# Performance work log

Hardware: AMD Instinct MI355X
Metric: run time of the kernel (lower is better)

The kernel has to match this reference:

```python
import jax, jax.numpy as jnp
import numpy as np

B, S = 1, 2048
D, HD, NH, NKV, L, V, FF = 2048, 256, 8, 4, 4, 32000, 8192
WINDOW = 1024
SOFTCAP = 50.0
FINAL_CAP = 30.0
EPS = 1e-6
THETA = 10000.0
ATTN_TYPES = ("local", "global", "local", "global")
NEG = -2.3819763e38
SCALE = HD ** -0.5


def _rms(x, w):
    # RMSNorm with unit offset: x * rsqrt(mean(x^2)+eps) * (1 + w)
    n = x * jax.lax.rsqrt(jnp.mean(x * x, axis=-1, keepdims=True) + EPS)
    return n * (1.0 + w)


def _rope(x, cos, sin):
    # x: [B, S, H, HD]; rotate-half formulation (Gemma pairs i with i+HD/2)
    h = HD // 2
    x1, x2 = x[..., :h], x[..., h:]
    c = cos[None, :, None, :]
    s = sin[None, :, None, :]
    return jnp.concatenate([x1 * c - x2 * s, x1 * s + x2 * c], axis=-1)


def setup_inputs() -> dict:
    key = jax.random.key(0)
    ks = jax.random.split(key, 15)
    sd = 0.02
    f = lambda k, shape: jax.random.normal(k, shape, jnp.float32) * sd
    return {
        "input_ids": jax.random.randint(ks[0], (B, S), 0, V),
        "embed": f(ks[1], (V, D)),
        "wq": f(ks[2], (L, NH * HD, D)),
        "wk": f(ks[3], (L, NKV * HD, D)),
        "wv": f(ks[4], (L, NKV * HD, D)),
        "wo": f(ks[5], (L, D, NH * HD)),
        "wg": f(ks[6], (L, FF, D)),
        "wu": f(ks[7], (L, FF, D)),
        "wd": f(ks[8], (L, D, FF)),
        "ln_in": f(ks[9], (L, D)),
        "ln_pa": f(ks[10], (L, D)),
        "ln_pf": f(ks[11], (L, D)),
        "ln_pff": f(ks[12], (L, D)),
        "ln_f": f(ks[13], (D,)),
        "w_lm": f(ks[14], (V, D)),
    }


def _forward(input_ids, embed, wq, wk, wv, wo, wg, wu, wd,
             ln_in, ln_pa, ln_pf, ln_pff, ln_f, w_lm):
    # rotary tables
    pos = jnp.arange(S, dtype=jnp.float32)
    inv = 1.0 / (THETA ** (jnp.arange(0, HD, 2, dtype=jnp.float32) / HD))
    ang = pos[:, None] * inv[None, :]
    cos, sin = jnp.cos(ang), jnp.sin(ang)  # [S, HD/2]

    # additive masks
    i = jnp.arange(S)[:, None]
    j = jnp.arange(S)[None, :]
    causal = jnp.where(j > i, NEG, 0.0).astype(jnp.float32)
    local = jnp.where((j > i) | (i - j >= WINDOW), NEG, 0.0).astype(jnp.float32)

    h = embed[input_ids] * jnp.asarray(D ** 0.5, jnp.float32)
    rep = NH // NKV
    for l in range(L):
        mask = local if ATTN_TYPES[l] == "local" else causal
        x = _rms(h, ln_in[l])
        q = jnp.einsum('bsd,od->bso', x, wq[l]).reshape(B, S, NH, HD)
        k = jnp.einsum('bsd,od->bso', x, wk[l]).reshape(B, S, NKV, HD)
        v = jnp.einsum('bsd,od->bso', x, wv[l]).reshape(B, S, NKV, HD)
        q = _rope(q, cos, sin)
        k = _rope(k, cos, sin)
        k = jnp.repeat(k, rep, axis=2)  # GQA expand
        v = jnp.repeat(v, rep, axis=2)
        q = q.transpose(0, 2, 1, 3)  # bhsd
        k = k.transpose(0, 2, 1, 3)
        v = v.transpose(0, 2, 1, 3)
        qk = jnp.einsum('bhsd,bhfd->bhsf', q, k) * SCALE
        qk = jnp.tanh(qk / SOFTCAP) * SOFTCAP  # attn logit softcap
        scores = jax.nn.softmax(qk + mask, axis=-1)
        a = jnp.einsum('bhsf,bhfd->bhsd', scores, v)
        a = a.transpose(0, 2, 1, 3).reshape(B, S, NH * HD)
        attn_out = jnp.einsum('bso,do->bsd', a, wo[l])
        h = h + _rms(attn_out, ln_pa[l])  # post-attn norm then residual
        x = _rms(h, ln_pf[l])
        gate = jax.nn.gelu(jnp.einsum('bsd,fd->bsf', x, wg[l]), approximate=True)
        up = jnp.einsum('bsd,fd->bsf', x, wu[l])
        mlp = jnp.einsum('bsf,df->bsd', gate * up, wd[l])
        h = h + _rms(mlp, ln_pff[l])
    h = _rms(h, ln_f)
    logits = jnp.einsum('bsd,vd->bsv', h, w_lm)
    return jnp.tanh(logits / FINAL_CAP) * FINAL_CAP


def reference(input_ids, embed, wq, wk, wv, wo, wg, wu, wd,
              ln_in, ln_pa, ln_pf, ln_pff, ln_f, w_lm):
    return _forward(input_ids, embed, wq, wk, wv, wo, wg, wu, wd,
                    ln_in, ln_pa, ln_pf, ln_pff, ln_f, w_lm)
```

## Files before the change

### kernel.cpp

```cpp
#include <hip/hip_runtime.h>
#include <hip/hip_bf16.h>

typedef __attribute__((ext_vector_type(8))) __bf16 bf16x8;
typedef __attribute__((ext_vector_type(4))) float floatx4;

typedef __attribute__((address_space(1))) const unsigned char kGlb;
typedef __attribute__((address_space(3))) unsigned char kLds;

static constexpr int S = 2048;
static constexpr int D = 2048;
static constexpr int HD = 256;
static constexpr int NH = 8;
static constexpr int NKV = 4;
static constexpr int NLAYER = 4;
static constexpr int VOCAB = 32000;
static constexpr int FF = 8192;
static constexpr int WINDOW = 1024;

__device__ __forceinline__ float blk_sum(float v) {
    __shared__ float sm[4];
    #pragma unroll
    for (int o = 32; o > 0; o >>= 1) v += __shfl_down(v, o, 64);
    int lane = threadIdx.x & 63, w = threadIdx.x >> 6;
    __syncthreads();
    if (lane == 0) sm[w] = v;
    __syncthreads();
    return sm[0] + sm[1] + sm[2] + sm[3];
}

__device__ __forceinline__ float blk_max(float v) {
    __shared__ float sm[4];
    #pragma unroll
    for (int o = 32; o > 0; o >>= 1) v = fmaxf(v, __shfl_down(v, o, 64));
    int lane = threadIdx.x & 63, w = threadIdx.x >> 6;
    __syncthreads();
    if (lane == 0) sm[w] = v;
    __syncthreads();
    return fmaxf(fmaxf(sm[0], sm[1]), fmaxf(sm[2], sm[3]));
}

__global__ void embed_kernel(const int* __restrict__ ids, const float* __restrict__ E,
                             float* __restrict__ h) {
    int d = blockIdx.x * 256 + threadIdx.x;
    int s = blockIdx.y;
    h[(long)s * D + d] = E[(long)ids[s] * D + d] * 45.25483399593904f;
}

__global__ void rope_table_kernel(float* __restrict__ c, float* __restrict__ sn) {
    int i = threadIdx.x;
    int p = blockIdx.x;
    float inv = powf(10000.f, -(float)i / 128.f);
    float a = (float)p * inv;
    c[p * 128 + i] = cosf(a);
    sn[p * 128 + i] = sinf(a);
}

__global__ void cvt_bf16_kernel(const float* __restrict__ src, __hip_bfloat16* __restrict__ dst,
                                long n8) {
    long stride = (long)gridDim.x * 256;
    for (long i = (long)blockIdx.x * 256 + threadIdx.x; i < n8; i += stride) {
        long o = i * 8;
        float4 a = *(const float4*)(src + o);
        float4 b = *(const float4*)(src + o + 4);
        __hip_bfloat16 h8[8] = {
            __float2bfloat16(a.x), __float2bfloat16(a.y),
            __float2bfloat16(a.z), __float2bfloat16(a.w),
            __float2bfloat16(b.x), __float2bfloat16(b.y),
            __float2bfloat16(b.z), __float2bfloat16(b.w)};
        *(uint4*)(dst + o) = *(const uint4*)h8;
    }
}

__global__ void cvt_inter_kernel(const float* __restrict__ src, __hip_bfloat16* __restrict__ dst,
                                 int half, long n8) {
    long stride = (long)gridDim.x * 256;
    for (long i = (long)blockIdx.x * 256 + threadIdx.x; i < n8; i += stride) {
        long o = i * 8;
        long row = o >> 11, col = o & 2047;
        float4 a = *(const float4*)(src + o);
        float4 b = *(const float4*)(src + o + 4);
        __hip_bfloat16 h8[8] = {
            __float2bfloat16(a.x), __float2bfloat16(a.y),
            __float2bfloat16(a.z), __float2bfloat16(a.w),
            __float2bfloat16(b.x), __float2bfloat16(b.y),
            __float2bfloat16(b.z), __float2bfloat16(b.w)};
        *(uint4*)(dst + ((row * 2 + half) << 11) + col) = *(const uint4*)h8;
    }
}

__global__ void rms_bf16_kernel(const float* __restrict__ h, const float* __restrict__ w,
                                __hip_bfloat16* __restrict__ o) {
    int s = blockIdx.x;
    const float* row = h + (long)s * D;
    float vals[8], ss = 0.f;
    #pragma unroll
    for (int t = 0; t < 8; ++t) {
        int j = t * 256 + threadIdx.x;
        float v = row[j]; vals[t] = v; ss += v * v;
    }
    ss = blk_sum(ss);
    float r = rsqrtf(ss * (1.f / D) + 1e-6f);
    #pragma unroll
    for (int t = 0; t < 8; ++t) {
        int j = t * 256 + threadIdx.x;
        o[(long)s * D + j] = __float2bfloat16(vals[t] * r * (1.f + w[j]));
    }
}

__global__ void resid_rms_kernel(float* __restrict__ h, const float* __restrict__ tt,
                                 const float* __restrict__ w) {
    int s = blockIdx.x;
    const float* row = tt + (long)s * D;
    float* hr = h + (long)s * D;
    float vals[8], ss = 0.f;
    #pragma unroll
    for (int t = 0; t < 8; ++t) {
        int j = t * 256 + threadIdx.x;
        float v = row[j]; vals[t] = v; ss += v * v;
    }
    ss = blk_sum(ss);
    float r = rsqrtf(ss * (1.f / D) + 1e-6f);
    #pragma unroll
    for (int t = 0; t < 8; ++t) {
        int j = t * 256 + threadIdx.x;
        hr[j] += vals[t] * r * (1.f + w[j]);
    }
}

__global__ void rope_kernel(__hip_bfloat16* __restrict__ x, const float* __restrict__ cb,
                            const float* __restrict__ sb, int ldx) {
    int s = blockIdx.x, hh = blockIdx.y, i = threadIdx.x;
    __hip_bfloat16* p = x + (long)s * ldx + hh * HD;
    float x1 = __bfloat162float(p[i]);
    float x2 = __bfloat162float(p[128 + i]);
    float c = cb[s * 128 + i], sn = sb[s * 128 + i];
    p[i]       = __float2bfloat16(x1 * c - x2 * sn);
    p[128 + i] = __float2bfloat16(x1 * sn + x2 * c);
}

__global__ void transpose_v_kernel(const __hip_bfloat16* __restrict__ v,
                                   __hip_bfloat16* __restrict__ vt, int ldv) {
    __shared__ ushort tile[64][65];
    int s0 = blockIdx.x * 64, d0 = blockIdx.y * 64, kv = blockIdx.z;
    const ushort* vin = (const ushort*)v;
    ushort* vout = (ushort*)vt;
    #pragma unroll
    for (int it = 0; it < 4; ++it) {
        int slot = it * 256 + threadIdx.x;
        int r = slot >> 4, c4 = (slot & 15) << 2;
        ushort4 x = *(const ushort4*)(vin + (long)(s0 + r) * ldv + kv * HD + d0 + c4);
        tile[r][c4] = x.x; tile[r][c4 + 1] = x.y; tile[r][c4 + 2] = x.z; tile[r][c4 + 3] = x.w;
    }
    __syncthreads();
    #pragma unroll
    for (int it = 0; it < 4; ++it) {
        int slot = it * 256 + threadIdx.x;
        int rr = slot >> 4, c4 = (slot & 15) << 2;
        ushort4 y;
        y.x = tile[c4][rr]; y.y = tile[c4 + 1][rr]; y.z = tile[c4 + 2][rr]; y.w = tile[c4 + 3][rr];
        *(ushort4*)(vout + (long)kv * HD * S + (long)(d0 + rr) * S + s0 + c4) = y;
    }
}

__global__ void softmax_kernel(const __hip_bfloat16* __restrict__ sc,
                               __hip_bfloat16* __restrict__ pr, int isLocal) {
    int i = blockIdx.x, hh = blockIdx.y;
    const __hip_bfloat16* row = sc + ((long)hh * S + i) * S;
    __hip_bfloat16* orow = pr + ((long)hh * S + i) * S;
    int lo = isLocal ? max(0, i - (WINDOW - 1)) : 0;
    float vals[8];
    float m = -3.0e38f;
    #pragma unroll
    for (int t = 0; t < 8; ++t) {
        int j = t * 256 + threadIdx.x;
        bool chunkAny = (t * 256 <= i) && (t * 256 + 255 >= lo);
        if (chunkAny) {
            bool valid = (j <= i) && (j >= lo);
            float v = tanhf(__bfloat162float(row[j]) * (0.0625f / 50.f)) * 50.f;
            vals[t] = valid ? v : -3.0e38f;
            m = fmaxf(m, vals[t]);
        } else {
            vals[t] = -3.0e38f;
        }
    }
    m = blk_max(m);
    float ps[8], ssum = 0.f;
    #pragma unroll
    for (int t = 0; t < 8; ++t) {
        float p = (vals[t] > -1.0e38f) ? __expf(vals[t] - m) : 0.f;
        ps[t] = p; ssum += p;
    }
    ssum = blk_sum(ssum);
    float inv = 1.f / ssum;
    #pragma unroll
    for (int t = 0; t < 8; ++t) {
        int j = t * 256 + threadIdx.x;
        orow[j] = __float2bfloat16(ps[t] * inv);
    }
}

__global__ void mul_gu_kernel(__hip_bfloat16* __restrict__ gu) {
    long idx = ((long)blockIdx.x * 256 + threadIdx.x) * 8;
    long s = idx >> 13;
    long f = idx & 8191;
    __hip_bfloat16* gp = gu + s * 16384 + f;
    const __hip_bfloat16* up = gu + s * 16384 + 8192 + f;
    uint4 gv = *(const uint4*)gp;
    uint4 uv = *(const uint4*)up;
    const __hip_bfloat16* gb = (const __hip_bfloat16*)&gv;
    const __hip_bfloat16* ub = (const __hip_bfloat16*)&uv;
    __hip_bfloat16 o[8];
    #pragma unroll
    for (int j = 0; j < 8; ++j)
        o[j] = __float2bfloat16(__bfloat162float(gb[j]) * __bfloat162float(ub[j]));
    *(uint4*)gp = *(const uint4*)o;
}

template<int EPI, int WM, int WN, int MI, int NI>
__global__ __launch_bounds__(WM*WN*64, 2) void gemm_pipe(
    const __hip_bfloat16* __restrict__ A, const __hip_bfloat16* __restrict__ B,
    void* __restrict__ Cv, int K, int lda, int ldb, int ldc,
    long aBatch, long bBatch, long cBatch, int bzDiv, int gx, int kMode) {
    constexpr int T  = WM * WN * 64;
    constexpr int BM = WM * MI * 16;
    constexpr int BN = WN * NI * 16;
    constexpr int AE = BM * 32;
    constexpr int BE = BN * 32;
    __shared__ __hip_bfloat16 lds[4][AE + BE];

    const int tid = threadIdx.x;
    const int nwg = gridDim.x;
    const int orig = blockIdx.x;
    const int wgid = (orig & 7) * (nwg >> 3) + (orig >> 3);
    const int bx = wgid % gx, by = wgid / gx;
    const int bz = blockIdx.z;

    int kstart = 0, kend = K;
    if (kMode == 1) { if (by > bx) return; }
    else if (kMode == 2) { if (by > bx || bx - by >= 9) return; }
    else if (kMode == 3) { kend = min(K, (bx + 1) * BM); }
    else if (kMode == 4) { kend = min(K, (bx + 1) * BM); kstart = max(0, (bx - 1024 / BM) * BM); }

    const __hip_bfloat16* Ab = A + (long)bz * aBatch + (long)bx * BM * lda;
    const __hip_bfloat16* Bb = B + (long)(bz / bzDiv) * bBatch + (long)by * BN * ldb;

    const int w = tid >> 6, l = tid & 63;
    const int wm = w / WN, wn = w % WN;
    const int wrow = wm * MI * 16, wcol = wn * NI * 16;
    const int fr = l & 15, g = l >> 4;
    const int sR = tid >> 2;
    const int sc = tid & 3;

    floatx4 acc[MI][NI] = {};
    bf16x8 bfv[NI];
    bf16x8 af[MI / 2];

    auto stageA = [&](int t, int buf) {
        const int k0 = kstart + t * 32;
        #pragma unroll
        for (int i = 0; i < 2; ++i) {
            int row = sR + i * (T / 4);
            int scol = ((sc ^ ((row >> 1) & 3)) << 3);
            __builtin_amdgcn_global_load_lds(
                (kGlb*)(Ab + (long)row * lda + k0 + scol),
                (kLds*)(&lds[buf][0] + tid * 8 + i * (T * 8)), 16, 0, 0);
        }
    };
    auto stageB = [&](int t, int buf) {
        const int k0 = kstart + t * 32;
        #pragma unroll
        for (int i = 0; i < 2; ++i) {
            int row = sR + i * (T / 4);
            int scol = ((sc ^ ((row >> 1) & 3)) << 3);
            __builtin_amdgcn_global_load_lds(
                (kGlb*)(Bb + (long)row * ldb + k0 + scol),
                (kLds*)(&lds[buf][AE] + tid * 8 + i * (T * 8)), 16, 0, 0);
        }
    };

    auto phase0 = [&](int buf, int t3, bool doStage) {
        const char* AsB = (const char*)&lds[buf][0];
        const char* BsB = (const char*)&lds[buf][AE];
        #pragma unroll
        for (int mi = 0; mi < MI / 2; ++mi) {
            int ra = wrow + mi * 16 + fr;
            af[mi] = *(const bf16x8*)(AsB + ra * 64 + ((g ^ ((ra >> 1) & 3)) << 4));
        }
        #pragma unroll
        for (int ni = 0; ni < NI; ++ni) {
            int rb = wcol + ni * 16 + fr;
            bfv[ni] = *(const bf16x8*)(BsB + rb * 64 + ((g ^ ((rb >> 1) & 3)) << 4));
        }
        if (doStage) stageA(t3, t3 & 3);
        __builtin_amdgcn_s_barrier();
        asm volatile("s_waitcnt lgkmcnt(0)" ::: "memory");
        __builtin_amdgcn_sched_barrier(0);
        __builtin_amdgcn_s_setprio(1);
        #pragma unroll
        for (int mi = 0; mi < MI / 2; ++mi)
            #pragma unroll
            for (int ni = 0; ni < NI; ++ni)
                acc[mi][ni] = __builtin_amdgcn_mfma_f32_16x16x32_bf16(af[mi], bfv[ni], acc[mi][ni], 0, 0, 0);
        __builtin_amdgcn_s_setprio(0);
        __builtin_amdgcn_sched_barrier(0);
        __builtin_amdgcn_s_barrier();
    };

    auto phase1 = [&](int buf, int t3, bool doStage, int vm) {
        const char* AsB = (const char*)&lds[buf][0];
        #pragma unroll
        for (int mi = 0; mi < MI / 2; ++mi) {
            int ra = wrow + (MI / 2 + mi) * 16 + fr;
            af[mi] = *(const bf16x8*)(AsB + ra * 64 + ((g ^ ((ra >> 1) & 3)) << 4));
        }
        if (doStage) stageB(t3, t3 & 3);
        if (vm == 8)      asm volatile("s_waitcnt vmcnt(8)" ::: "memory");
        else if (vm == 4) asm volatile("s_waitcnt vmcnt(4)" ::: "memory");
        else if (vm == 0) asm volatile("s_waitcnt vmcnt(0)" ::: "memory");
        __builtin_amdgcn_s_barrier();
        asm volatile("s_waitcnt lgkmcnt(0)" ::: "memory");
        __builtin_amdgcn_sched_barrier(0);
        __builtin_amdgcn_s_setprio(1);
        #pragma unroll
        for (int mi = 0; mi < MI / 2; ++mi)
            #pragma unroll
            for (int ni = 0; ni < NI; ++ni)
                acc[MI / 2 + mi][ni] = __builtin_amdgcn_mfma_f32_16x16x32_bf16(af[mi], bfv[ni], acc[MI / 2 + mi][ni], 0, 0, 0);
        __builtin_amdgcn_s_setprio(0);
        __builtin_amdgcn_sched_barrier(0);
        __builtin_amdgcn_s_barrier();
    };

    const int nt = (kend - kstart) >> 5;
    stageA(0, 0); stageB(0, 0);
    stageA(1, 1); stageB(1, 1);
    stageA(2, 2); stageB(2, 2);
    asm volatile("s_waitcnt vmcnt(8)" ::: "memory");
    __builtin_amdgcn_s_barrier();

    for (int t = 0; t < nt - 3; ++t) {
        const int b = t & 3;
        phase0(b, t + 3, true);
        phase1(b, t + 3, true, 8);
    }
    phase0((nt - 3) & 3, 0, false); phase1((nt - 3) & 3, 0, false, 4);
    phase0((nt - 2) & 3, 0, false); phase1((nt - 2) & 3, 0, false, 0);
    phase0((nt - 1) & 3, 0, false); phase1((nt - 1) & 3, 0, false, -1);

    const long cBase = (long)bz * cBatch + (long)bx * BM * ldc + (long)by * BN;
    const int rg = (l >> 4) * 4;
    #pragma unroll
    for (int mi = 0; mi < MI; ++mi) {
        #pragma unroll
        for (int ni = 0; ni < NI; ++ni) {
            #pragma unroll
            for (int r = 0; r < 4; ++r) {
                int row = wrow + mi * 16 + rg + r;
                int col = wcol + ni * 16 + fr;
                float v = acc[mi][ni][r];
                if constexpr (EPI == 5) {
                    float pv = __shfl_xor(v, 1);
                    if (!(fr & 1)) {
                        float gg = 0.5f * v * (1.f + tanhf(0.7978845608f * (v + 0.044715f * v * v * v)));
                        long idx5 = ((long)bx * BM + row) * (long)ldc + (long)by * (BN / 2) + (col >> 1);
                        ((__hip_bfloat16*)Cv)[idx5] = __float2bfloat16(gg * pv);
                    }
                } else {
                    long idx = cBase + (long)row * ldc + col;
                    if constexpr (EPI == 0) {
                        ((float*)Cv)[idx] = v;
                    } else if constexpr (EPI == 1) {
                        ((__hip_bfloat16*)Cv)[idx] = __float2bfloat16(v);
                    } else if constexpr (EPI == 3) {
                        ((float*)Cv)[idx] = tanhf(v * (1.f / 30.f)) * 30.f;
                    }
                }
            }
        }
    }
}

template<int EPI>
__global__ __launch_bounds__(256) void gemm_f32w(
    const __hip_bfloat16* __restrict__ A, const float* __restrict__ Bv,
    void* __restrict__ Cv, int K, int lda, int ldb, int ldc) {
    __shared__ __hip_bfloat16 As[128][32];
    __shared__ __hip_bfloat16 Bs[128][32];
    const int tid = threadIdx.x;
    const __hip_bfloat16* Ab = A + (long)blockIdx.x * 128 * lda;
    const float* Bb = Bv + (long)blockIdx.y * 128 * ldb;
    const int wid = tid >> 6, lane = tid & 63;
    const int wr = (wid >> 1) * 64, wc = (wid & 1) * 64;
    const int fr = lane & 15;
    const int kb = (lane >> 4) * 8;
    floatx4 acc[4][4] = {};
    for (int k0 = 0; k0 < K; k0 += 32) {
        __syncthreads();
        #pragma unroll
        for (int it = 0; it < 2; ++it) {
            int slot = tid + it * 256;
            int r = slot >> 2, c8 = (slot & 3) * 8;
            *reinterpret_cast<uint4*>(&As[r][c8]) =
                *reinterpret_cast<const uint4*>(Ab + (long)r * lda + k0 + c8);
        }
        #pragma unroll
        for (int it = 0; it < 4; ++it) {
            int slot = tid + it * 256;
            int r = slot >> 3, c4 = (slot & 7) * 4;
            float4 f = *reinterpret_cast<const float4*>(Bb + (long)r * ldb + k0 + c4);
            __hip_bfloat16 t4[4] = {__float2bfloat16(f.x), __float2bfloat16(f.y),
                                    __float2bfloat16(f.z), __float2bfloat16(f.w)};
            *reinterpret_cast<ushort4*>(&Bs[r][c4]) = *reinterpret_cast<const ushort4*>(t4);
        }
        __syncthreads();
        bf16x8 af[4], bfr[4];
        #pragma unroll
        for (int i = 0; i < 4; ++i)
            af[i] = *reinterpret_cast<const bf16x8*>(&As[wr + i * 16 + fr][kb]);
        #pragma unroll
        for (int j = 0; j < 4; ++j)
            bfr[j] = *reinterpret_cast<const bf16x8*>(&Bs[wc + j * 16 + fr][kb]);
        #pragma unroll
        for (int i = 0; i < 4; ++i)
            #pragma unroll
            for (int j = 0; j < 4; ++j)
                acc[i][j] = __builtin_amdgcn_mfma_f32_16x16x32_bf16(af[i], bfr[j], acc[i][j], 0, 0, 0);
    }
    const long cTile = (long)blockIdx.x * 128 * ldc + (long)blockIdx.y * 128;
    const int rg = (lane >> 4) * 4;
    #pragma unroll
    for (int i = 0; i < 4; ++i)
        #pragma unroll
        for (int j = 0; j < 4; ++j)
            #pragma unroll
            for (int r = 0; r < 4; ++r) {
                int row = wr + i * 16 + rg + r;
                int col = wc + j * 16 + fr;
                long idx = cTile + (long)row * ldc + col;
                float v = acc[i][j][r];
                if constexpr (EPI == 0) ((float*)Cv)[idx] = v;
                else if constexpr (EPI == 1) ((__hip_bfloat16*)Cv)[idx] = __float2bfloat16(v);
                else if constexpr (EPI == 2) {
                    float gg = 0.5f * v * (1.f + tanhf(0.7978845608f * (v + 0.044715f * v * v * v)));
                    ((__hip_bfloat16*)Cv)[idx] = __float2bfloat16(gg);
                } else ((float*)Cv)[idx] = tanhf(v * (1.f / 30.f)) * 30.f;
            }
}

extern "C" void kernel_launch(void* const* d_in, const int* in_sizes, int n_in,
                              void* d_out, int out_size, void* d_ws, size_t ws_size,
                              hipStream_t stream) {
    const int*   ids    = (const int*)d_in[0];
    const float* embedW = (const float*)d_in[1];
    const float* wq     = (const float*)d_in[2];
    const float* wk     = (const float*)d_in[3];
    const float* wv     = (const float*)d_in[4];
    const float* wo     = (const float*)d_in[5];
    const float* wg     = (const float*)d_in[6];
    const float* wu     = (const float*)d_in[7];
    const float* wd     = (const float*)d_in[8];
    const float* ln_in  = (const float*)d_in[9];
    const float* ln_pa  = (const float*)d_in[10];
    const float* ln_pf  = (const float*)d_in[11];
    const float* ln_pff = (const float*)d_in[12];
    const float* ln_f   = (const float*)d_in[13];
    const float* w_lm   = (const float*)d_in[14];
    float* out = (float*)d_out;

    char* ws = (char*)d_ws;
    size_t off = 0;
    auto alloc = [&](size_t bytes) -> void* {
        size_t o = (off + 255) & ~(size_t)255;
        off = o + bytes;
        return (void*)(ws + o);
    };

    float* h            = (float*)alloc((size_t)S * D * 4);
    __hip_bfloat16* xb  = (__hip_bfloat16*)alloc((size_t)S * D * 2);
    __hip_bfloat16* qkvb = (__hip_bfloat16*)alloc((size_t)S * 4096 * 2);
    __hip_bfloat16* vT  = (__hip_bfloat16*)alloc((size_t)NKV * HD * S * 2);
    __hip_bfloat16* ab  = (__hip_bfloat16*)alloc((size_t)S * NH * HD * 2);
    float* tmpf         = (float*)alloc((size_t)S * D * 4);
    __hip_bfloat16* guP = (__hip_bfloat16*)alloc((size_t)S * FF * 2);
    __hip_bfloat16* gu  = (__hip_bfloat16*)alloc((size_t)S * 16384 * 2);
    float* cosb         = (float*)alloc((size_t)S * 128 * 4);
    float* sinb         = (float*)alloc((size_t)S * 128 * 4);
    __hip_bfloat16* scores = (__hip_bfloat16*)alloc((size_t)NH * S * S * 2);
    __hip_bfloat16* probs  = (__hip_bfloat16*)alloc((size_t)NH * S * S * 2);

    const long SLq = 2048L * 2048, SLkv = 1024L * 2048, SLff = 8192L * 2048;
    const long nWlm = (long)VOCAB * D;
    __hip_bfloat16* wqkvb = (__hip_bfloat16*)alloc(4L * 4096 * 2048 * 2);
    __hip_bfloat16* wgub  = (__hip_bfloat16*)alloc(4L * 16384 * 2048 * 2);
    __hip_bfloat16* wob   = (__hip_bfloat16*)alloc(4L * SLq * 2);
    __hip_bfloat16* wdb   = (__hip_bfloat16*)alloc(4L * SLff * 2);
    __hip_bfloat16* wlmb  = (__hip_bfloat16*)alloc(nWlm * 2);
    const bool big = (off <= ws_size);
    (void)in_sizes; (void)n_in; (void)out_size;

    rope_table_kernel<<<dim3(S), dim3(128), 0, stream>>>(cosb, sinb);
    embed_kernel<<<dim3(D / 256, S), dim3(256), 0, stream>>>(ids, embedW, h);

    auto cvt = [&](const float* s, __hip_bfloat16* dp, long n) {
        long n8 = n / 8;
        long want = (n8 + 255) / 256;
        int blocks = (int)(want < 2048 ? want : 2048);
        cvt_bf16_kernel<<<dim3(blocks), dim3(256), 0, stream>>>(s, dp, n8);
    };
    auto cvtI = [&](const float* s, __hip_bfloat16* dp, int half, long n) {
        long n8 = n / 8;
        long want = (n8 + 255) / 256;
        int blocks = (int)(want < 2048 ? want : 2048);
        cvt_inter_kernel<<<dim3(blocks), dim3(256), 0, stream>>>(s, dp, half, n8);
    };
    if (big) {
        for (int l = 0; l < NLAYER; ++l) {
            cvt(wq + l * SLq,  wqkvb + (size_t)l * 4096 * 2048,                SLq);
            cvt(wk + l * SLkv, wqkvb + (size_t)l * 4096 * 2048 + 2048L * 2048, SLkv);
            cvt(wv + l * SLkv, wqkvb + (size_t)l * 4096 * 2048 + 3072L * 2048, SLkv);
            cvtI(wg + l * SLff, wgub + (size_t)l * 16384 * 2048, 0, SLff);
            cvtI(wu + l * SLff, wgub + (size_t)l * 16384 * 2048, 1, SLff);
        }
        cvt(wo, wob, 4L * SLq);
        cvt(wd, wdb, 4L * SLff);
        cvt(w_lm, wlmb, nWlm);
    }

    auto p256 = [&](int epi, const __hip_bfloat16* A, const __hip_bfloat16* B, void* C,
                    int K, int lda, int ldb, int ldc, int gx, int gy) {
        dim3 grid(gx * gy, 1, 1);
        if (epi == 3)
            gemm_pipe<3, 2, 4, 8, 4><<<grid, 512, 0, stream>>>(A, B, C, K, lda, ldb, ldc, 0, 0, 0, 1, gx, 0);
        else
            gemm_pipe<5, 2, 4, 8, 4><<<grid, 512, 0, stream>>>(A, B, C, K, lda, ldb, ldc, 0, 0, 0, 1, gx, 0);
    };
    auto p128 = [&](int epi, const __hip_bfloat16* A, const __hip_bfloat16* B, void* C,
                    int K, int lda, int ldb, int ldc, int gx, int gy, int gz,
                    long aB, long bB, long cB, int bzDiv, int kMode) {
        dim3 grid(gx * gy, 1, gz);
        switch (epi) {
        case 0: gemm_pipe<0, 2, 2, 4, 4><<<grid, 256, 0, stream>>>(A, B, C, K, lda, ldb, ldc, aB, bB, cB, bzDiv, gx, kMode); break;
        default: gemm_pipe<1, 2, 2, 4, 4><<<grid, 256, 0, stream>>>(A, B, C, K, lda, ldb, ldc, aB, bB, cB, bzDiv, gx, kMode); break;
        }
    };

    for (int l = 0; l < NLAYER; ++l) {
        int isLocal = (l % 2 == 0) ? 1 : 0;
        rms_bf16_kernel<<<dim3(S), dim3(256), 0, stream>>>(h, ln_in + l * D, xb);
        if (big) {
            p128(1, xb, wqkvb + (size_t)l * 4096 * 2048, qkvb, D, D, D, 4096, 16, 32, 1, 0, 0, 0, 1, 0);
        } else {
            gemm_f32w<1><<<dim3(16, 16), 256, 0, stream>>>(xb, wq + l * SLq, qkvb, D, D, D, 4096);
            gemm_f32w<1><<<dim3(16, 8), 256, 0, stream>>>(xb, wk + l * SLkv, qkvb + 2048, D, D, D, 4096);
            gemm_f32w<1><<<dim3(16, 8), 256, 0, stream>>>(xb, wv + l * SLkv, qkvb + 3072, D, D, D, 4096);
        }
        rope_kernel<<<dim3(S, NH), dim3(128), 0, stream>>>(qkvb, cosb, sinb, 4096);
        rope_kernel<<<dim3(S, NKV), dim3(128), 0, stream>>>(qkvb + 2048, cosb, sinb, 4096);
        transpose_v_kernel<<<dim3(S / 64, HD / 64, NKV), 256, 0, stream>>>(qkvb + 3072, vT, 4096);
        p128(1, qkvb, qkvb + 2048, scores, HD, 4096, 4096, S, 16, 16, NH,
             (long)HD, (long)HD, (long)S * S, 2, isLocal ? 2 : 1);
        softmax_kernel<<<dim3(S, NH), dim3(256), 0, stream>>>(scores, probs, isLocal);
        p128(1, probs, vT, ab, S, S, S, NH * HD, 16, 2, NH,
             (long)S * S, (long)HD * S, (long)HD, 2, isLocal ? 4 : 3);
        if (big) {
            p128(0, ab, wob + (size_t)l * SLq, tmpf, NH * HD, NH * HD, NH * HD, D, 16, 16, 1, 0, 0, 0, 1, 0);
        } else {
            gemm_f32w<0><<<dim3(16, 16), 256, 0, stream>>>(ab, wo + l * SLq, tmpf, NH * HD, NH * HD, NH * HD, D);
        }
        resid_rms_kernel<<<dim3(S), dim3(256), 0, stream>>>(h, tmpf, ln_pa + l * D);
        rms_bf16_kernel<<<dim3(S), dim3(256), 0, stream>>>(h, ln_pf + l * D, xb);
        if (big) {
            p256(5, xb, wgub + (size_t)l * 16384 * 2048, guP, D, D, D, FF, 8, 64);
        } else {
            gemm_f32w<2><<<dim3(16, 64), 256, 0, stream>>>(xb, wg + l * SLff, gu, D, D, D, 16384);
            gemm_f32w<1><<<dim3(16, 64), 256, 0, stream>>>(xb, wu + l * SLff, gu + 8192, D, D, D, 16384);
            mul_gu_kernel<<<dim3((S * FF) / (256 * 8)), 256, 0, stream>>>(gu);
        }
        if (big) {
            p128(0, guP, wdb + (size_t)l * SLff, tmpf, FF, FF, FF, D, 16, 16, 1, 0, 0, 0, 1, 0);
        } else {
            gemm_f32w<0><<<dim3(16, 16), 256, 0, stream>>>(gu, wd + l * SLff, tmpf, FF, 16384, FF, D);
        }
        resid_rms_kernel<<<dim3(S), dim3(256), 0, stream>>>(h, tmpf, ln_pff + l * D);
    }

    rms_bf16_kernel<<<dim3(S), dim3(256), 0, stream>>>(h, ln_f, xb);
    if (big) {
        p256(3, xb, wlmb, out, D, D, D, VOCAB, 8, VOCAB / 256);
    } else {
        gemm_f32w<3><<<dim3(16, VOCAB / 128), 256, 0, stream>>>(xb, w_lm, out, D, D, D, VOCAB);
    }
}
```

Baseline: 2.594 ms.

## Add 8-phase 256x256 GEMM kernel for MLP gate/up and LM head

Adds a new 256x256-tile GEMM kernel that splits each tile into four 128x128 quadrants and interleaves LDS fragment reads, async global-to-LDS staging and MFMA bursts across eight barrier-separated phases per two K-steps. It uses s_setprio around the MFMA bursts and explicit vmcnt waits. The aim is to hide global and LDS latency behind matrix work for the large GEMMs, which are the fused gate/up with GELU-multiply epilogue and the softcapped LM head. In exchange there are many more barriers per iteration, and the 128 KB of LDS per block may limit occupancy to a single block per CU despite the launch bound of 2. The old gemm_pipe drops its now-unused epilogues.

```diff
diff --git a/kernel.cpp b/kernel.cpp
--- a/kernel.cpp
+++ b/kernel.cpp
@@ -216,6 +216,181 @@
     *(uint4*)gp = *(const uint4*)o;
 }
 
+#define RD_AF(BUF, HALF)                                                          \
+    {                                                                             \
+        const char* _p = (const char*)&ldsA[BUF][HALF][0];                        \
+        _Pragma("unroll")                                                         \
+        for (int mi = 0; mi < 4; ++mi) {                                          \
+            int r = wm * 64 + mi * 16 + fr;                                       \
+            _Pragma("unroll")                                                     \
+            for (int ks = 0; ks < 2; ++ks) {                                      \
+                int c = ks * 4 + g;                                               \
+                af[mi][ks] = *(const bf16x8*)(_p + r * 128 + ((c ^ (r & 7)) << 4)); \
+            }                                                                     \
+        }                                                                         \
+    }
+
+#define RD_BF(DST, BUF, HALF)                                                     \
+    {                                                                             \
+        const char* _p = (const char*)&ldsB[BUF][HALF][0];                        \
+        _Pragma("unroll")                                                         \
+        for (int ni = 0; ni < 2; ++ni) {                                          \
+            int r = wn * 32 + ni * 16 + fr;                                       \
+            _Pragma("unroll")                                                     \
+            for (int ks = 0; ks < 2; ++ks) {                                      \
+                int c = ks * 4 + g;                                               \
+                DST[ni][ks] = *(const bf16x8*)(_p + r * 128 + ((c ^ (r & 7)) << 4)); \
+            }                                                                     \
+        }                                                                         \
+    }
+
+#define MM(QM, QN, BF)                                                            \
+    __builtin_amdgcn_s_setprio(1);                                                \
+    _Pragma("unroll")                                                             \
+    for (int mi = 0; mi < 4; ++mi)                                                \
+        _Pragma("unroll")                                                         \
+        for (int ni = 0; ni < 2; ++ni)                                            \
+            _Pragma("unroll")                                                     \
+            for (int ks = 0; ks < 2; ++ks)                                        \
+                acc[QM][QN][mi][ni] = __builtin_amdgcn_mfma_f32_16x16x32_bf16(    \
+                    af[mi][ks], BF[ni][ks], acc[QM][QN][mi][ni], 0, 0, 0);        \
+    __builtin_amdgcn_s_setprio(0);
+
+#define PH_TAIL                                                                   \
+    __builtin_amdgcn_s_barrier();                                                 \
+    asm volatile("s_waitcnt lgkmcnt(0)" ::: "memory");                            \
+    __builtin_amdgcn_sched_barrier(0);
+
+#define PH_END                                                                    \
+    __builtin_amdgcn_sched_barrier(0);                                            \
+    __builtin_amdgcn_s_barrier();
+
+template<int EPI>
+__global__ __launch_bounds__(512, 2) void gemm_8ph(
+    const __hip_bfloat16* __restrict__ A, const __hip_bfloat16* __restrict__ B,
+    void* __restrict__ Cv, int K, int lda, int ldb, int ldc, int gx) {
+    __shared__ __hip_bfloat16 ldsA[2][2][8192];
+    __shared__ __hip_bfloat16 ldsB[2][2][8192];
+    const int tid = threadIdx.x;
+    const int nwg = gridDim.x;
+    const int orig = blockIdx.x;
+    const int wgid = (orig & 7) * (nwg >> 3) + (orig >> 3);
+    const int bx = wgid % gx, by = wgid / gx;
+
+    const __hip_bfloat16* Ab = A + (long)bx * 256 * lda;
+    const __hip_bfloat16* Bb = B + (long)by * 256 * ldb;
+
+    const int w = tid >> 6, l = tid & 63;
+    const int wm = w >> 2, wn = w & 3;
+    const int fr = l & 15, g = l >> 4;
+    const int sRow0 = tid >> 3;
+    const int sCh = tid & 7;
+
+    floatx4 acc[2][2][4][2] = {};
+    bf16x8 af[4][2], bf0[2][2], bf1[2][2];
+
+    auto stage = [&](const __hip_bfloat16* src, int ld, int k0, __hip_bfloat16* dst) {
+        #pragma unroll
+        for (int i = 0; i < 2; ++i) {
+            int row = sRow0 + i * 64;
+            int cs = (sCh ^ (row & 7)) * 8;
+            __builtin_amdgcn_global_load_lds(
+                (kGlb*)(src + (long)row * ld + k0 + cs),
+                (kLds*)((char*)dst + i * 8192 + tid * 16), 16, 0, 0);
+        }
+    };
+
+    const int nt = K >> 6;
+    const int niter = nt >> 1;
+
+    stage(Ab,             lda, 0,  &ldsA[0][0][0]);
+    stage(Bb,             ldb, 0,  &ldsB[0][0][0]);
+    stage(Ab + 128 * lda, lda, 0,  &ldsA[0][1][0]);
+    stage(Bb + 128 * ldb, ldb, 0,  &ldsB[0][1][0]);
+    stage(Ab,             lda, 64, &ldsA[1][0][0]);
+    stage(Bb,             ldb, 64, &ldsB[1][0][0]);
+    asm volatile("s_waitcnt vmcnt(4)" ::: "memory");
+    __builtin_amdgcn_s_barrier();
+
+    for (int it = 0; it < niter; ++it) {
+        const int t = it * 2;
+        const bool last = (it == niter - 1);
+        const int kN1 = (t + 1) * 64;
+        const int kN2 = (t + 2) * 64;
+        const int kN3 = (t + 3) * 64;
+        RD_AF(0, 0);
+        RD_BF(bf0, 0, 0);
+        stage(Ab + 128 * lda, lda, kN1, &ldsA[1][1][0]);
+        PH_TAIL
+        MM(0, 0, bf0)
+        PH_END
+        RD_BF(bf1, 0, 1);
+        stage(Bb + 128 * ldb, ldb, kN1, &ldsB[1][1][0]);
+        PH_TAIL
+        MM(0, 1, bf1)
+        PH_END
+        RD_AF(0, 1);
+        if (!last) stage(Ab, lda, kN2, &ldsA[0][0][0]);
+        PH_TAIL
+        MM(1, 0, bf0)
+        PH_END
+        if (!last) stage(Bb, ldb, kN2, &ldsB[0][0][0]);
+        MM(1, 1, bf1)
+        __builtin_amdgcn_sched_barrier(0);
+        if (last) { asm volatile("s_waitcnt vmcnt(0)" ::: "memory"); }
+        else      { asm volatile("s_waitcnt vmcnt(4)" ::: "memory"); }
+        __builtin_amdgcn_s_barrier();
+        RD_AF(1, 0);
+        RD_BF(bf0, 1, 0);
+        if (!last) stage(Ab + 128 * lda, lda, kN2, &ldsA[0][1][0]);
+        PH_TAIL
+        MM(0, 0, bf0)
+        PH_END
+        RD_BF(bf1, 1, 1);
+        if (!last) stage(Bb + 128 * ldb, ldb, kN2, &ldsB[0][1][0]);
+        PH_TAIL
+        MM(0, 1, bf1)
+        PH_END
+        RD_AF(1, 1);
+        if (!last) stage(Ab, lda, kN3, &ldsA[1][0][0]);
+        PH_TAIL
+        MM(1, 0, bf0)
+        PH_END
+        if (!last) stage(Bb, ldb, kN3, &ldsB[1][0][0]);
+        MM(1, 1, bf1)
+        __builtin_amdgcn_sched_barrier(0);
+        if (!last) { asm volatile("s_waitcnt vmcnt(4)" ::: "memory"); }
+        __builtin_amdgcn_s_barrier();
+    }
+
+    const long cBase = (long)bx * 256 * ldc + (long)by * 256;
+    const int rg = (l >> 4) * 4;
+    #pragma unroll
+    for (int qm = 0; qm < 2; ++qm)
+    #pragma unroll
+    for (int qn = 0; qn < 2; ++qn)
+    #pragma unroll
+    for (int mi = 0; mi < 4; ++mi)
+    #pragma unroll
+    for (int ni = 0; ni < 2; ++ni)
+    #pragma unroll
+    for (int r = 0; r < 4; ++r) {
+        int row = qm * 128 + wm * 64 + mi * 16 + rg + r;
+        int col = qn * 128 + wn * 32 + ni * 16 + fr;
+        float v = acc[qm][qn][mi][ni][r];
+        if constexpr (EPI == 3) {
+            ((float*)Cv)[cBase + (long)row * ldc + col] = tanhf(v * (1.f / 30.f)) * 30.f;
+        } else {
+            float pv = __shfl_xor(v, 1);
+            if (!(fr & 1)) {
+                float gg = 0.5f * v * (1.f + tanhf(0.7978845608f * (v + 0.044715f * v * v * v)));
+                long idx5 = ((long)bx * 256 + row) * (long)ldc + (long)by * 128 + (col >> 1);
+                ((__hip_bfloat16*)Cv)[idx5] = __float2bfloat16(gg * pv);
+            }
+        }
+    }
+}
+
 template<int EPI, int WM, int WN, int MI, int NI>
 __global__ __launch_bounds__(WM*WN*64, 2) void gemm_pipe(
     const __hip_bfloat16* __restrict__ A, const __hip_bfloat16* __restrict__ B,
@@ -357,23 +532,12 @@
             for (int r = 0; r < 4; ++r) {
                 int row = wrow + mi * 16 + rg + r;
                 int col = wcol + ni * 16 + fr;
+                long idx = cBase + (long)row * ldc + col;
                 float v = acc[mi][ni][r];
-                if constexpr (EPI == 5) {
-                    float pv = __shfl_xor(v, 1);
-                    if (!(fr & 1)) {
-                        float gg = 0.5f * v * (1.f + tanhf(0.7978845608f * (v + 0.044715f * v * v * v)));
-                        long idx5 = ((long)bx * BM + row) * (long)ldc + (long)by * (BN / 2) + (col >> 1);
-                        ((__hip_bfloat16*)Cv)[idx5] = __float2bfloat16(gg * pv);
-                    }
+                if constexpr (EPI == 0) {
+                    ((float*)Cv)[idx] = v;
                 } else {
-                    long idx = cBase + (long)row * ldc + col;
-                    if constexpr (EPI == 0) {
-                        ((float*)Cv)[idx] = v;
-                    } else if constexpr (EPI == 1) {
-                        ((__hip_bfloat16*)Cv)[idx] = __float2bfloat16(v);
-                    } else if constexpr (EPI == 3) {
-                        ((float*)Cv)[idx] = tanhf(v * (1.f / 30.f)) * 30.f;
-                    }
+                    ((__hip_bfloat16*)Cv)[idx] = __float2bfloat16(v);
                 }
             }
         }
@@ -530,9 +694,9 @@
                     int K, int lda, int ldb, int ldc, int gx, int gy) {
         dim3 grid(gx * gy, 1, 1);
         if (epi == 3)
-            gemm_pipe<3, 2, 4, 8, 4><<<grid, 512, 0, stream>>>(A, B, C, K, lda, ldb, ldc, 0, 0, 0, 1, gx, 0);
+            gemm_8ph<3><<<grid, 512, 0, stream>>>(A, B, C, K, lda, ldb, ldc, gx);
         else
-            gemm_pipe<5, 2, 4, 8, 4><<<grid, 512, 0, stream>>>(A, B, C, K, lda, ldb, ldc, 0, 0, 0, 1, gx, 0);
+            gemm_8ph<5><<<grid, 512, 0, stream>>>(A, B, C, K, lda, ldb, ldc, gx);
     };
     auto p128 = [&](int epi, const __hip_bfloat16* A, const __hip_bfloat16* B, void* C,
                     int K, int lda, int ldb, int ldc, int gx, int gy, int gz,
```

New measurement: 2.573 ms. Within noise of the previous version (-0.8%).
